# Kernel optimization log

Hardware: AMD Instinct MI355X
Metric: run time of the kernel (lower is better)

The kernel has to match this reference:

```python
import jax, jax.numpy as jnp
import numpy as np
from jax import lax

NC = 32
EPS = 1e-12


def unfold3x3(x):
    # x: [B,C,H,W] -> [B, C*9, H*W], matching F.unfold(kernel=3, padding=1)
    B, C, H, W = x.shape
    xp = jnp.pad(x, ((0, 0), (0, 0), (1, 1), (1, 1)))
    patches = jnp.stack([xp[:, :, i:i + H, j:j + W]
                         for i in range(3) for j in range(3)], axis=2)  # [B,C,9,H,W]
    return patches.reshape(B, C * 9, H * W)


def fold3x3(u, H, W):
    # u: [B, C*9, H*W] -> [B, C, H, W], matching F.fold(kernel=3, padding=1)
    B = u.shape[0]
    C = u.shape[1] // 9
    p = u.reshape(B, C, 3, 3, H, W)
    out = jnp.zeros((B, C, H + 2, W + 2), u.dtype)
    for i in range(3):
        for j in range(3):
            out = out.at[:, :, i:i + H, j:j + W].add(p[:, :, i, j])
    return out[:, :, 1:H + 1, 1:W + 1]


def l2norm(x, axis):
    n = jnp.sqrt(jnp.sum(x * x, axis=axis, keepdims=True))
    return x / jnp.maximum(n, EPS)


def conv3x3(x, w, b):
    y = lax.conv_general_dilated(x, w, (1, 1), 'SAME',
                                 dimension_numbers=('NCHW', 'OIHW', 'NCHW'))
    return y + b[None, :, None, None]


def setup_inputs() -> dict:
    key = jax.random.key(0)
    k = jax.random.split(key, 6)
    B, C, H, W = 2, NC, 80, 80
    in_HSI = jax.random.normal(k[0], (B, C, H, W), jnp.float32)
    in_PAN = jax.random.normal(k[1], (B, C, H, W), jnp.float32)
    fan1 = 2 * C * 9
    fan2 = C * 9
    w1 = jax.random.normal(k[2], (C, 2 * C, 3, 3), jnp.float32) / np.sqrt(fan1)
    b1 = jax.random.normal(k[3], (C,), jnp.float32) * 0.01
    w2 = jax.random.normal(k[4], (C, C, 3, 3), jnp.float32) / np.sqrt(fan2)
    b2 = jax.random.normal(k[5], (C,), jnp.float32) * 0.01
    return {"in_HSI": in_HSI, "in_PAN": in_PAN, "w1": w1, "b1": b1, "w2": w2, "b2": b2}


def reference(in_HSI, in_PAN, w1, b1, w2, b2):
    B, C, H, W = in_HSI.shape
    L = H * W
    HSI_unfold = unfold3x3(in_HSI)                      # [B, C*9, L]
    PAN_unfold = unfold3x3(in_PAN)                      # [B, C*9, L]
    PAN_q = l2norm(jnp.transpose(PAN_unfold, (0, 2, 1)), axis=2)  # [B, L, C*9]
    HSI_k = l2norm(HSI_unfold, axis=1)                  # [B, C*9, L]
    R = jnp.einsum('blc,bcm->blm', PAN_q, HSI_k)        # [B, L, L]
    R_star = jnp.max(R, axis=1)                         # [B, L]
    R_arg = jnp.argmax(R, axis=1)                       # [B, L]
    # gather columns of unfold(in_PAN) selected by 1-NN indices
    T_unfold = jnp.take_along_axis(PAN_unfold, R_arg[:, None, :], axis=2)
    T_lv3 = fold3x3(T_unfold, H, W) / 9.0               # [B, C, H, W]
    S = R_star.reshape(B, 1, H, W)
    h = jax.nn.relu(conv3x3(jnp.concatenate([T_lv3, in_HSI], axis=1), w1, b1))
    res = conv3x3(h, w2, b2) * S + in_HSI
    return res
```

## Files before the change

kernel.cpp:

```cpp
#include <hip/hip_runtime.h>
#include <hip/hip_bf16.h>
#include <hip/hip_fp16.h>
#include <stdint.h>

#define HH 80
#define WW 80
#define LL 6400
#define CC 32
#define BB 2
#define COG 8
#define DELTA 0.011f
#define NT8 800

typedef __bf16 bf16x8 __attribute__((ext_vector_type(8)));
typedef float  f32x4  __attribute__((ext_vector_type(4)));

__device__ __forceinline__ int div80(int v) {
    return (int)(((unsigned)v * 52429u) >> 22);
}

__device__ __forceinline__ unsigned short f2bf(float f) {
    unsigned int u = __float_as_uint(f);
    return (unsigned short)((u + 0x7fffu + ((u >> 16) & 1u)) >> 16);
}

__device__ __forceinline__ void gload_lds16(const void* g, void* l) {
    __builtin_amdgcn_global_load_lds(
        (const __attribute__((address_space(1))) void*)g,
        (__attribute__((address_space(3))) void*)l, 16, 0, 0);
}

__global__ __launch_bounds__(256) void fusedunf_kernel(const float* __restrict__ HSI,
                                                       const float* __restrict__ PAN,
                                                       float* __restrict__ invH,
                                                       float* __restrict__ invP,
                                                       float* __restrict__ PANunf,
                                                       float* __restrict__ HSIunf,
                                                       char* __restrict__ Apack,
                                                       char* __restrict__ Bpack) {
    __shared__ float simg[CC][3][82];
    __shared__ float sinv[80];
    const int y = blockIdx.x, mat = blockIdx.y, b = blockIdx.z;
    const int tid = threadIdx.x;
    const float* img = (mat ? HSI : PAN) + (size_t)b * CC * LL;

    for (int i = tid; i < CC * 3; i += 256) {
        simg[i / 3][i % 3][0] = 0.f;
        simg[i / 3][i % 3][81] = 0.f;
    }
    for (int i = tid; i < CC * 3 * 80; i += 256) {
        int c = i / 240, r = i - c * 240;
        int dy = r / 80, x = r - dy * 80;
        int yy = y + dy - 1;
        float v = ((unsigned)yy < 80u) ? img[(size_t)c * LL + yy * 80 + x] : 0.f;
        simg[c][dy][x + 1] = v;
    }
    __syncthreads();

    if (tid < 80) {
        float s = 0.f;
        #pragma unroll 4
        for (int c = 0; c < CC; ++c)
            #pragma unroll
            for (int dy = 0; dy < 3; ++dy)
                #pragma unroll
                for (int dx = 0; dx < 3; ++dx) {
                    float v = simg[c][dy][tid + dx];
                    s = fmaf(v, v, s);
                }
        float inv = 1.f / fmaxf(sqrtf(s), 1e-12f);
        sinv[tid] = inv;
        (mat ? invH : invP)[b * LL + y * 80 + tid] = inv;
    }
    __syncthreads();

    {
        float* unfBase = (mat ? HSIunf : PANunf) + ((size_t)b * LL + y * 80) * 288;
        for (int i = tid; i < 5760; i += 256) {
            const int fidx = i * 4;
            const int l = fidx / 288, k = fidx - l * 288;
            float4 v;
            {
                int kk = k;     int c = kk / 9, t = kk - c * 9; v.x = simg[c][t / 3][l + t % 3];
                kk = k + 1;     c = kk / 9; t = kk - c * 9;     v.y = simg[c][t / 3][l + t % 3];
                kk = k + 2;     c = kk / 9; t = kk - c * 9;     v.z = simg[c][t / 3][l + t % 3];
                kk = k + 3;     c = kk / 9; t = kk - c * 9;     v.w = simg[c][t / 3][l + t % 3];
            }
            *(float4*)(unfBase + fidx) = v;
        }
    }

    {
        char* pk = mat ? Bpack : Apack;
        for (int i = tid; i < 2880; i += 256) {
            const int l = i / 36, g = i - l * 36;
            const float inv = sinv[l];
            unsigned short hs[8];
            #pragma unroll
            for (int jj = 0; jj < 8; ++jj) {
                int kk = g * 8 + jj;
                int c = kk / 9, t = kk - c * 9;
                hs[jj] = f2bf(simg[c][t / 3][l + t % 3] * inv);
            }
            const int q = g / 12;
            const int slot = (g % 12) ^ (l & 15);
            size_t off = ((size_t)(b * 3 + q) * LL + y * 80 + l) * 256 + slot * 16;
            uint4 hv;
            hv.x = hs[0] | ((unsigned)hs[1] << 16); hv.y = hs[2] | ((unsigned)hs[3] << 16);
            hv.z = hs[4] | ((unsigned)hs[5] << 16); hv.w = hs[6] | ((unsigned)hs[7] << 16);
            *(uint4*)(pk + off) = hv;
        }
    }
}

__global__ __launch_bounds__(256, 1) void simq_kernel(const char* __restrict__ Apack,
                                                      const char* __restrict__ Bpack,
                                                      __half* __restrict__ tileMax8,
                                                      __half* __restrict__ tileMax64) {
    __shared__ __align__(16) char Alds[2][32768];
    __shared__ __align__(16) char Blds[98304];
    const int orig = blockIdx.x;
    const int xcd = orig & 7, idx = orig >> 3;
    const int wg = (xcd < 4 ? xcd * 63 : 252 + (xcd - 4) * 62) + idx;
    const int b = wg / 250;
    int rest = wg - b * 250;
    const int sp = rest / 50;
    const int mt = rest - sp * 50;

    const int tid = threadIdx.x;
    const int lane = tid & 63, w = tid >> 6;
    const int wl = w >> 1, wm = w & 1;
    const int r15 = lane & 15, h = lane >> 4;
    const char* Ab = Apack + (size_t)b * 3 * LL * 256;
    const char* Bb = Bpack + (size_t)b * 3 * LL * 256;
    const int m0 = mt * 128;
    const f32x4 fzero = {0.f, 0.f, 0.f, 0.f};

    int gp[3];
    #pragma unroll
    for (int ks = 0; ks < 3; ++ks) gp[ks] = ((ks * 4 + h) ^ r15) * 16;

    #pragma unroll 1
    for (int it = 0; it < 24; ++it) {
        const int i = it * 256 + tid;
        const int pl = i >> 11;
        const int off = (i & 2047) * 16;
        gload_lds16(Bb + ((size_t)pl * LL + m0) * 256 + off, Blds + i * 16);
    }

    const char* gAbase = Ab + w * 8192 + lane * 16;
    char* lA0 = Alds[0] + w * 8192;
    char* lA1 = Alds[1] + w * 8192;

    {
        const char* gA = gAbase + ((size_t)(sp * 10) * 128) * 256;
        #pragma unroll
        for (int i = 0; i < 8; ++i) gload_lds16(gA + i * 1024, lA0 + i * 1024);
    }

    const char* Bw = Blds + (wm * 64 + r15) * 256;
    int cur = 0;
    #pragma unroll 1
    for (int lt = 0; lt < 10; ++lt) {
        const int l0 = (sp * 10 + lt) * 128;
        f32x4 acc[4][4];
        #pragma unroll
        for (int i = 0; i < 4; ++i)
            #pragma unroll
            for (int j = 0; j < 4; ++j) acc[i][j] = fzero;

        #pragma unroll
        for (int c = 0; c < 3; ++c) {
            if (c < 2 || lt < 9) {
                const int c2  = (c + 1) % 3;
                const int l0n = (c == 2) ? l0 + 128 : l0;
                const char* gA = gAbase + ((size_t)c2 * LL + l0n) * 256;
                char* lA = (cur ^ 1) ? lA1 : lA0;
                #pragma unroll
                for (int i = 0; i < 8; ++i) gload_lds16(gA + i * 1024, lA + i * 1024);
                asm volatile("s_waitcnt vmcnt(8)" ::: "memory");
            } else {
                asm volatile("s_waitcnt vmcnt(0)" ::: "memory");
            }
            __builtin_amdgcn_s_barrier();
            asm volatile("" ::: "memory");
            const char* lAr = Alds[cur];
            const char* lBc = Bw + c * 32768;
            #pragma unroll
            for (int ks = 0; ks < 3; ++ks) {
                bf16x8 af[4], bfr[4];
                #pragma unroll
                for (int f = 0; f < 4; ++f) {
                    af[f]  = *(const bf16x8*)(lAr + (wl * 64 + f * 16 + r15) * 256 + gp[ks]);
                    bfr[f] = *(const bf16x8*)(lBc + (f * 16) * 256 + gp[ks]);
                }
                #pragma unroll
                for (int fl = 0; fl < 4; ++fl)
                    #pragma unroll
                    for (int fm = 0; fm < 4; ++fm)
                        acc[fl][fm] = __builtin_amdgcn_mfma_f32_16x16x32_bf16(
                            af[fl], bfr[fm], acc[fl][fm], 0, 0, 0);
            }
            asm volatile("s_waitcnt lgkmcnt(0)" ::: "memory");
            __builtin_amdgcn_s_barrier();
            asm volatile("" ::: "memory");
            cur ^= 1;
        }

        const int T64 = (sp * 10 + lt) * 2 + wl;
        #pragma unroll
        for (int fm = 0; fm < 4; ++fm) {
            float m4[4];
            #pragma unroll
            for (int fl = 0; fl < 4; ++fl) {
                f32x4 a = acc[fl][fm];
                m4[fl] = fmaxf(fmaxf(a[0], a[1]), fmaxf(a[2], a[3]));
            }
            const int m = m0 + wm * 64 + fm * 16 + r15;
            #pragma unroll
            for (int fl = 0; fl < 4; ++fl) {
                float v = fmaxf(m4[fl], __shfl_xor(m4[fl], 16, 64));
                if ((h & 1) == 0)
                    tileMax8[((size_t)b * LL + m) * NT8 + T64 * 8 + fl * 2 + (h >> 1)] = __float2half(v);
            }
            float vA = fmaxf(fmaxf(m4[0], m4[1]), fmaxf(m4[2], m4[3]));
            vA = fmaxf(vA, __shfl_xor(vA, 16, 64));
            vA = fmaxf(vA, __shfl_xor(vA, 32, 64));
            if (h == 0)
                tileMax64[((size_t)b * LL + m) * 100 + T64] = __float2half(vA);
        }
    }
}

__global__ __launch_bounds__(256) void scanfix_kernel(const float* __restrict__ PANunf,
                                                      const float* __restrict__ HSIunf,
                                                      const float* __restrict__ invH,
                                                      const float* __restrict__ invP,
                                                      const __half* __restrict__ tileMax8,
                                                      const __half* __restrict__ tileMax64,
                                                      float* __restrict__ Sv, int* __restrict__ Sa) {
    const int orig = blockIdx.x;
    const int swz = (orig & 7) * 400 + (orig >> 3);
    const int gw = swz * 4 + (threadIdx.x >> 6);
    const int lane = threadIdx.x & 63;
    const int b = gw / LL;
    const __half* tm64 = tileMax64 + (size_t)gw * 100;
    const __half* tm8  = tileMax8  + (size_t)gw * NT8;

    float t64[2];
    #pragma unroll
    for (int i = 0; i < 2; ++i) {
        int T = i * 64 + lane;
        t64[i] = (T < 100) ? __half2float(tm64[T]) : -3.0e38f;
    }
    float v1 = fmaxf(t64[0], t64[1]);
    #pragma unroll
    for (int d = 1; d < 64; d <<= 1) v1 = fmaxf(v1, __shfl_xor(v1, d, 64));
    const float th = v1 - DELTA;

    const float ihm = invH[gw];
    const int lql = lane >> 3, kq = lane & 7;

    float hreg[36];
    {
        const float4* hv4 = (const float4*)(HSIunf + (size_t)gw * 288 + kq * 36);
        #pragma unroll
        for (int j = 0; j < 9; ++j) {
            float4 v = hv4[j];
            hreg[j * 4 + 0] = v.x; hreg[j * 4 + 1] = v.y;
            hreg[j * 4 + 2] = v.z; hreg[j * 4 + 3] = v.w;
        }
    }

    float bv = -3.0e38f; int bl = 0x7fffffff;

    #pragma unroll 1
    for (int i = 0; i < 2; ++i) {
        unsigned long long mask = __ballot(t64[i] >= th);
        while (mask) {
            const int t = __ffsll((long long)mask) - 1;
            mask &= mask - 1;
            const int T64 = i * 64 + t;
            float s8 = __half2float(tm8[T64 * 8 + (lane & 7)]);
            unsigned sub = (unsigned)(__ballot(s8 >= th) & 0xffull);
            while (sub) {
                const int j = __ffs(sub) - 1;
                sub &= sub - 1;
                const int T = T64 * 8 + j;
                const int l = T * 8 + lql;
                const float4* pv4 = (const float4*)(PANunf + ((size_t)b * LL + l) * 288 + kq * 36);
                float part = 0.f;
                #pragma unroll
                for (int jj = 0; jj < 9; ++jj) {
                    float4 p = pv4[jj];
                    part = fmaf(p.x, hreg[jj * 4 + 0], part);
                    part = fmaf(p.y, hreg[jj * 4 + 1], part);
                    part = fmaf(p.z, hreg[jj * 4 + 2], part);
                    part = fmaf(p.w, hreg[jj * 4 + 3], part);
                }
                part += __shfl_xor(part, 1, 64);
                part += __shfl_xor(part, 2, 64);
                part += __shfl_xor(part, 4, 64);
                const float val = part * invP[b * LL + l] * ihm;
                if (val > bv || (val == bv && l < bl)) { bv = val; bl = l; }
            }
        }
    }
    #pragma unroll
    for (int d = 1; d < 64; d <<= 1) {
        float ov = __shfl_xor(bv, d, 64);
        int   ol = __shfl_xor(bl, d, 64);
        if (ov > bv || (ov == bv && ol < bl)) { bv = ov; bl = ol; }
    }
    if (lane == 0) { Sv[gw] = bv; Sa[gw] = bl; }
}

__global__ void tfold_kernel(const float* __restrict__ PAN, const int* __restrict__ Sa,
                             float* __restrict__ T) {
    int g = blockIdx.x * blockDim.x + threadIdx.x;
    if (g >= BB * CC * LL) return;
    int bc = g / LL, l = g - bc * LL;
    int b = bc >> 5;
    int y = div80(l), x = l - y * 80;
    const float* img = PAN + (size_t)bc * LL;
    const int* Sab = Sa + b * LL;
    float acc = 0.f;
    #pragma unroll
    for (int i = 0; i < 3; ++i) {
        int yp = y + 1 - i;
        if ((unsigned)yp >= 80u) continue;
        #pragma unroll
        for (int j = 0; j < 3; ++j) {
            int xp = x + 1 - j;
            if ((unsigned)xp >= 80u) continue;
            int a = Sab[yp * 80 + xp];
            int ya = div80(a), xa = a - ya * 80;
            int py = ya + i - 1, px = xa + j - 1;
            if ((unsigned)py < 80u && (unsigned)px < 80u) acc += img[py * 80 + px];
        }
    }
    T[g] = acc * (1.f / 9.f);
}

__global__ __launch_bounds__(256) void conv1_kernel(const float* __restrict__ T,
                                                    const float* __restrict__ HSI,
                                                    const float* __restrict__ w1,
                                                    const float* __restrict__ b1,
                                                    float* __restrict__ h) {
    __shared__ __align__(16) float wl[64][9][COG];
    const int tid = threadIdx.x;
    const int co0 = blockIdx.y * COG;
    for (int idx = tid; idx < 64 * 9 * COG; idx += 256) {
        int cog = idx & (COG - 1);
        int rest = idx >> 3;
        int cin = rest / 9, tap = rest - cin * 9;
        wl[cin][tap][cog] = w1[(co0 + cog) * (64 * 9) + cin * 9 + tap];
    }
    __syncthreads();
    const int g = blockIdx.x * 256 + tid;
    const int b = g / LL, l = g - b * LL;
    const int y = div80(l), x = l - y * 80;
    float acc[COG];
    #pragma unroll
    for (int i = 0; i < COG; ++i) acc[i] = 0.f;
    for (int cin = 0; cin < 64; ++cin) {
        const float* img = (cin < CC) ? (T + (size_t)(b * CC + cin) * LL)
                                      : (HSI + (size_t)(b * CC + (cin - CC)) * LL);
        float tap[9];
        #pragma unroll
        for (int i = 0; i < 3; ++i)
            #pragma unroll
            for (int j = 0; j < 3; ++j) {
                int yy = y + i - 1, xx = x + j - 1;
                tap[i * 3 + j] = ((unsigned)yy < 80u && (unsigned)xx < 80u) ? img[yy * 80 + xx] : 0.f;
            }
        #pragma unroll
        for (int t9 = 0; t9 < 9; ++t9) {
            const float4 wa = *reinterpret_cast<const float4*>(&wl[cin][t9][0]);
            const float4 wb = *reinterpret_cast<const float4*>(&wl[cin][t9][4]);
            acc[0] = fmaf(tap[t9], wa.x, acc[0]);
            acc[1] = fmaf(tap[t9], wa.y, acc[1]);
            acc[2] = fmaf(tap[t9], wa.z, acc[2]);
            acc[3] = fmaf(tap[t9], wa.w, acc[3]);
            acc[4] = fmaf(tap[t9], wb.x, acc[4]);
            acc[5] = fmaf(tap[t9], wb.y, acc[5]);
            acc[6] = fmaf(tap[t9], wb.z, acc[6]);
            acc[7] = fmaf(tap[t9], wb.w, acc[7]);
        }
    }
    #pragma unroll
    for (int cog = 0; cog < COG; ++cog) {
        float v = acc[cog] + b1[co0 + cog];
        h[(size_t)(b * CC + co0 + cog) * LL + l] = fmaxf(v, 0.f);
    }
}

__global__ __launch_bounds__(256) void conv2_kernel(const float* __restrict__ hbuf,
                                                    const float* __restrict__ HSI,
                                                    const float* __restrict__ Sv,
                                                    const float* __restrict__ w2,
                                                    const float* __restrict__ b2,
                                                    float* __restrict__ out) {
    __shared__ __align__(16) float wl[CC][9][COG];
    const int tid = threadIdx.x;
    const int co0 = blockIdx.y * COG;
    for (int idx = tid; idx < CC * 9 * COG; idx += 256) {
        int cog = idx & (COG - 1);
        int rest = idx >> 3;
        int cin = rest / 9, tap = rest - cin * 9;
        wl[cin][tap][cog] = w2[(co0 + cog) * (CC * 9) + cin * 9 + tap];
    }
    __syncthreads();
    const int g = blockIdx.x * 256 + tid;
    const int b = g / LL, l = g - b * LL;
    const int y = div80(l), x = l - y * 80;
    float acc[COG];
    #pragma unroll
    for (int i = 0; i < COG; ++i) acc[i] = 0.f;
    for (int cin = 0; cin < CC; ++cin) {
        const float* img = hbuf + (size_t)(b * CC + cin) * LL;
        float tap[9];
        #pragma unroll
        for (int i = 0; i < 3; ++i)
            #pragma unroll
            for (int j = 0; j < 3; ++j) {
                int yy = y + i - 1, xx = x + j - 1;
                tap[i * 3 + j] = ((unsigned)yy < 80u && (unsigned)xx < 80u) ? img[yy * 80 + xx] : 0.f;
            }
        #pragma unroll
        for (int t9 = 0; t9 < 9; ++t9) {
            const float4 wa = *reinterpret_cast<const float4*>(&wl[cin][t9][0]);
            const float4 wb = *reinterpret_cast<const float4*>(&wl[cin][t9][4]);
            acc[0] = fmaf(tap[t9], wa.x, acc[0]);
            acc[1] = fmaf(tap[t9], wa.y, acc[1]);
            acc[2] = fmaf(tap[t9], wa.z, acc[2]);
            acc[3] = fmaf(tap[t9], wa.w, acc[3]);
            acc[4] = fmaf(tap[t9], wb.x, acc[4]);
            acc[5] = fmaf(tap[t9], wb.y, acc[5]);
            acc[6] = fmaf(tap[t9], wb.z, acc[6]);
            acc[7] = fmaf(tap[t9], wb.w, acc[7]);
        }
    }
    const float s = Sv[b * LL + l];
    #pragma unroll
    for (int cog = 0; cog < COG; ++cog) {
        int c = co0 + cog;
        out[(size_t)(b * CC + c) * LL + l] = fmaf(acc[cog] + b2[c], s, HSI[(size_t)(b * CC + c) * LL + l]);
    }
}

extern "C" void kernel_launch(void* const* d_in, const int* in_sizes, int n_in,
                              void* d_out, int out_size, void* d_ws, size_t ws_size,
                              hipStream_t stream) {
    const float* HSI = (const float*)d_in[0];
    const float* PAN = (const float*)d_in[1];
    const float* w1  = (const float*)d_in[2];
    const float* b1  = (const float*)d_in[3];
    const float* w2  = (const float*)d_in[4];
    const float* b2  = (const float*)d_in[5];
    float* out = (float*)d_out;

    char* ws = (char*)d_ws;
    size_t off = 0;
    auto alloc = [&](size_t bytes) -> void* {
        void* p = ws + off;
        off += (bytes + 255) & ~(size_t)255;
        return p;
    };
    float* invH  = (float*)alloc((size_t)BB * LL * 4);
    float* invP  = (float*)alloc((size_t)BB * LL * 4);
    char*  Apack = (char*) alloc((size_t)BB * 3 * LL * 256);
    char*  Bpack = (char*) alloc((size_t)BB * 3 * LL * 256);
    __half* tileMax8  = (__half*)alloc((size_t)BB * LL * NT8 * 2);
    __half* tileMax64 = (__half*)alloc((size_t)BB * LL * 100 * 2);
    float* PANunf = (float*)alloc((size_t)BB * LL * 288 * 4);
    float* HSIunf = (float*)alloc((size_t)BB * LL * 288 * 4);
    float* Sv    = (float*)alloc((size_t)BB * LL * 4);
    int*   Sa    = (int*)  alloc((size_t)BB * LL * 4);
    float* T     = (float*)alloc((size_t)BB * CC * LL * 4);
    float* hbuf  = (float*)alloc((size_t)BB * CC * LL * 4);

    fusedunf_kernel<<<dim3(80, 2, BB), 256, 0, stream>>>(HSI, PAN, invH, invP,
                                                         PANunf, HSIunf, Apack, Bpack);
    simq_kernel<<<dim3(500), 256, 0, stream>>>(Apack, Bpack, tileMax8, tileMax64);
    scanfix_kernel<<<dim3(BB * LL / 4), 256, 0, stream>>>(PANunf, HSIunf, invH, invP,
                                                          tileMax8, tileMax64, Sv, Sa);
    tfold_kernel<<<dim3((BB * CC * LL + 255) / 256), 256, 0, stream>>>(PAN, Sa, T);
    conv1_kernel<<<dim3(BB * LL / 256, CC / COG), 256, 0, stream>>>(T, HSI, w1, b1, hbuf);
    conv2_kernel<<<dim3(BB * LL / 256, CC / COG), 256, 0, stream>>>(hbuf, HSI, Sv, w2, b2, out);
}
```

Before: 255.5 us.

## Hold B operand in registers in simq kernel and widen conv output-channel groups

The simq GEMM kernel stops staging the B tile (96KB) in LDS and instead loads each wave's B fragments once into registers, which cuts LDS use so two workgroups can share a CU (launch bounds raised to 2). The per-k-step LDS reads for B go away. Separately, the conv kernels now compute 16 output channels per thread instead of 8, halving the grid in y and reusing each tap load across more FMAs. The trade-off is much higher register pressure: 36 bf16x8 B fragments per thread in simq, and 16 accumulators in the convs, which risks spills or lower occupancy.

```diff
diff --git a/kernel.cpp b/kernel.cpp
--- a/kernel.cpp
+++ b/kernel.cpp
@@ -8,7 +8,7 @@
 #define LL 6400
 #define CC 32
 #define BB 2
-#define COG 8
+#define COG 16
 #define DELTA 0.011f
 #define NT8 800
 
@@ -113,12 +113,11 @@
     }
 }
 
-__global__ __launch_bounds__(256, 1) void simq_kernel(const char* __restrict__ Apack,
+__global__ __launch_bounds__(256, 2) void simq_kernel(const char* __restrict__ Apack,
                                                       const char* __restrict__ Bpack,
                                                       __half* __restrict__ tileMax8,
                                                       __half* __restrict__ tileMax64) {
     __shared__ __align__(16) char Alds[2][32768];
-    __shared__ __align__(16) char Blds[98304];
     const int orig = blockIdx.x;
     const int xcd = orig & 7, idx = orig >> 3;
     const int wg = (xcd < 4 ? xcd * 63 : 252 + (xcd - 4) * 62) + idx;
@@ -136,16 +135,18 @@
     const int m0 = mt * 128;
     const f32x4 fzero = {0.f, 0.f, 0.f, 0.f};
 
-    int gp[3];
-    #pragma unroll
-    for (int ks = 0; ks < 3; ++ks) gp[ks] = ((ks * 4 + h) ^ r15) * 16;
-
-    #pragma unroll 1
-    for (int it = 0; it < 24; ++it) {
-        const int i = it * 256 + tid;
-        const int pl = i >> 11;
-        const int off = (i & 2047) * 16;
-        gload_lds16(Bb + ((size_t)pl * LL + m0) * 256 + off, Blds + i * 16);
+    bf16x8 bq[3][3][4];
+    {
+        const int rowb = m0 + wm * 64 + r15;
+        #pragma unroll
+        for (int c = 0; c < 3; ++c)
+            #pragma unroll
+            for (int ks = 0; ks < 3; ++ks)
+                #pragma unroll
+                for (int fm = 0; fm < 4; ++fm) {
+                    const int gp = ((ks * 4 + h) ^ r15) * 16;
+                    bq[c][ks][fm] = *(const bf16x8*)(Bb + ((size_t)c * LL + rowb + fm * 16) * 256 + gp);
+                }
     }
 
     const char* gAbase = Ab + w * 8192 + lane * 16;
@@ -158,7 +159,6 @@
         for (int i = 0; i < 8; ++i) gload_lds16(gA + i * 1024, lA0 + i * 1024);
     }
 
-    const char* Bw = Blds + (wm * 64 + r15) * 256;
     int cur = 0;
     #pragma unroll 1
     for (int lt = 0; lt < 10; ++lt) {
@@ -185,21 +185,19 @@
             __builtin_amdgcn_s_barrier();
             asm volatile("" ::: "memory");
             const char* lAr = Alds[cur];
-            const char* lBc = Bw + c * 32768;
             #pragma unroll
             for (int ks = 0; ks < 3; ++ks) {
-                bf16x8 af[4], bfr[4];
-                #pragma unroll
-                for (int f = 0; f < 4; ++f) {
-                    af[f]  = *(const bf16x8*)(lAr + (wl * 64 + f * 16 + r15) * 256 + gp[ks]);
-                    bfr[f] = *(const bf16x8*)(lBc + (f * 16) * 256 + gp[ks]);
-                }
+                const int gp = ((ks * 4 + h) ^ r15) * 16;
+                bf16x8 af[4];
+                #pragma unroll
+                for (int f = 0; f < 4; ++f)
+                    af[f] = *(const bf16x8*)(lAr + (wl * 64 + f * 16 + r15) * 256 + gp);
                 #pragma unroll
                 for (int fl = 0; fl < 4; ++fl)
                     #pragma unroll
                     for (int fm = 0; fm < 4; ++fm)
                         acc[fl][fm] = __builtin_amdgcn_mfma_f32_16x16x32_bf16(
-                            af[fl], bfr[fm], acc[fl][fm], 0, 0, 0);
+                            af[fl], bq[c][ks][fm], acc[fl][fm], 0, 0, 0);
             }
             asm volatile("s_waitcnt lgkmcnt(0)" ::: "memory");
             __builtin_amdgcn_s_barrier();
@@ -352,7 +350,7 @@
     const int co0 = blockIdx.y * COG;
     for (int idx = tid; idx < 64 * 9 * COG; idx += 256) {
         int cog = idx & (COG - 1);
-        int rest = idx >> 3;
+        int rest = idx >> 4;
         int cin = rest / 9, tap = rest - cin * 9;
         wl[cin][tap][cog] = w1[(co0 + cog) * (64 * 9) + cin * 9 + tap];
     }
@@ -376,16 +374,14 @@
             }
         #pragma unroll
         for (int t9 = 0; t9 < 9; ++t9) {
-            const float4 wa = *reinterpret_cast<const float4*>(&wl[cin][t9][0]);
-            const float4 wb = *reinterpret_cast<const float4*>(&wl[cin][t9][4]);
-            acc[0] = fmaf(tap[t9], wa.x, acc[0]);
-            acc[1] = fmaf(tap[t9], wa.y, acc[1]);
-            acc[2] = fmaf(tap[t9], wa.z, acc[2]);
-            acc[3] = fmaf(tap[t9], wa.w, acc[3]);
-            acc[4] = fmaf(tap[t9], wb.x, acc[4]);
-            acc[5] = fmaf(tap[t9], wb.y, acc[5]);
-            acc[6] = fmaf(tap[t9], wb.z, acc[6]);
-            acc[7] = fmaf(tap[t9], wb.w, acc[7]);
+            #pragma unroll
+            for (int q4 = 0; q4 < COG / 4; ++q4) {
+                const float4 wv = *reinterpret_cast<const float4*>(&wl[cin][t9][q4 * 4]);
+                acc[q4 * 4 + 0] = fmaf(tap[t9], wv.x, acc[q4 * 4 + 0]);
+                acc[q4 * 4 + 1] = fmaf(tap[t9], wv.y, acc[q4 * 4 + 1]);
+                acc[q4 * 4 + 2] = fmaf(tap[t9], wv.z, acc[q4 * 4 + 2]);
+                acc[q4 * 4 + 3] = fmaf(tap[t9], wv.w, acc[q4 * 4 + 3]);
+            }
         }
     }
     #pragma unroll
@@ -406,7 +402,7 @@
     const int co0 = blockIdx.y * COG;
     for (int idx = tid; idx < CC * 9 * COG; idx += 256) {
         int cog = idx & (COG - 1);
-        int rest = idx >> 3;
+        int rest = idx >> 4;
         int cin = rest / 9, tap = rest - cin * 9;
         wl[cin][tap][cog] = w2[(co0 + cog) * (CC * 9) + cin * 9 + tap];
     }
@@ -429,16 +425,14 @@
             }
         #pragma unroll
         for (int t9 = 0; t9 < 9; ++t9) {
-            const float4 wa = *reinterpret_cast<const float4*>(&wl[cin][t9][0]);
-            const float4 wb = *reinterpret_cast<const float4*>(&wl[cin][t9][4]);
-            acc[0] = fmaf(tap[t9], wa.x, acc[0]);
-            acc[1] = fmaf(tap[t9], wa.y, acc[1]);
-            acc[2] = fmaf(tap[t9], wa.z, acc[2]);
-            acc[3] = fmaf(tap[t9], wa.w, acc[3]);
-            acc[4] = fmaf(tap[t9], wb.x, acc[4]);
-            acc[5] = fmaf(tap[t9], wb.y, acc[5]);
-            acc[6] = fmaf(tap[t9], wb.z, acc[6]);
-            acc[7] = fmaf(tap[t9], wb.w, acc[7]);
+            #pragma unroll
+            for (int q4 = 0; q4 < COG / 4; ++q4) {
+                const float4 wv = *reinterpret_cast<const float4*>(&wl[cin][t9][q4 * 4]);
+                acc[q4 * 4 + 0] = fmaf(tap[t9], wv.x, acc[q4 * 4 + 0]);
+                acc[q4 * 4 + 1] = fmaf(tap[t9], wv.y, acc[q4 * 4 + 1]);
+                acc[q4 * 4 + 2] = fmaf(tap[t9], wv.z, acc[q4 * 4 + 2]);
+                acc[q4 * 4 + 3] = fmaf(tap[t9], wv.w, acc[q4 * 4 + 3]);
+            }
         }
     }
     const float s = Sv[b * LL + l];
```

New measurement: 256.5 us. Within noise of the previous version (+0.4%).
